# Kernel optimization log

Measured on AMD Instinct MI355X. Metric: run time of the kernel, lower is better.

Reference implementation:

```python
import jax, jax.numpy as jnp
import numpy as np

ALPHA = 0.1  # blend factor from init

def grid_sample_bilinear(tex, grid):
    # tex: [B,C,H,W]; grid: [B,Ho,Wo,2] with (x,y) in [-1,1].
    # Matches torch F.grid_sample(mode='bilinear', padding_mode='zeros', align_corners=False).
    B, C, H, W = tex.shape
    Ho, Wo = grid.shape[1], grid.shape[2]
    ix = ((grid[..., 0] + 1.0) * W - 1.0) * 0.5
    iy = ((grid[..., 1] + 1.0) * H - 1.0) * 0.5
    x0 = jnp.floor(ix); y0 = jnp.floor(iy)
    x1 = x0 + 1.0;      y1 = y0 + 1.0
    wx1 = ix - x0; wx0 = 1.0 - wx1
    wy1 = iy - y0; wy0 = 1.0 - wy1
    flat = tex.reshape(B, C, H * W).transpose(0, 2, 1)  # [B, H*W, C]

    def gather(xf, yf):
        valid = ((xf >= 0) & (xf < W) & (yf >= 0) & (yf < H)).astype(tex.dtype)
        xi = jnp.clip(xf.astype(jnp.int32), 0, W - 1)
        yi = jnp.clip(yf.astype(jnp.int32), 0, H - 1)
        idx = (yi * W + xi).reshape(B, Ho * Wo)
        v = jnp.take_along_axis(flat, idx[:, :, None], axis=1)  # [B, N, C]
        return v * valid.reshape(B, Ho * Wo)[:, :, None]

    w00 = (wx0 * wy0).reshape(B, -1)[:, :, None]
    w10 = (wx1 * wy0).reshape(B, -1)[:, :, None]
    w01 = (wx0 * wy1).reshape(B, -1)[:, :, None]
    w11 = (wx1 * wy1).reshape(B, -1)[:, :, None]
    out = (gather(x0, y0) * w00 + gather(x1, y0) * w10 +
           gather(x0, y1) * w01 + gather(x1, y1) * w11)  # [B, N, C]
    return out.reshape(B, Ho, Wo, C).transpose(0, 3, 1, 2)

def bicubic_grid_sample(tex, grid):
    # 5-tap Catmull-Rom approximation of bicubic filtering (matches BiCubicGridSample).
    B, C, H, W = tex.shape
    wsz = jnp.asarray([W, H], dtype=tex.dtype)
    rws = 1.0 / wsz
    uv = (grid + 1.0) * 0.5
    pos = uv * wsz
    cpos = jnp.floor(pos - 0.5) + 0.5
    f = pos - cpos; f2 = f * f; f3 = f2 * f
    w0 = -0.5 * f3 + f2 - 0.5 * f
    w1 = 1.5 * f3 - 2.5 * f2 + 1.0
    w2 = -1.5 * f3 + 2.0 * f2 + 0.5 * f
    w3 = 0.5 * f3 - 0.5 * f2
    w12 = w1 + w2
    tc12 = rws * (cpos + w2 / w12)
    tc0 = rws * (cpos - 1.0)
    tc3 = rws * (cpos + 2.0)

    def samp(u, v):
        uvg = jnp.stack((u, v), axis=-1)
        return grid_sample_bilinear(tex, (uvg - 0.5) * 2.0)  # UVToGrid

    # 5 taps in the plus pattern, with the per-tap scalar weights (alpha channel is a
    # constant 1 in the original, so the denominator is just the sum of the weights).
    k1 = w12[..., 0] * w0[..., 1]
    k2 = w0[..., 0] * w12[..., 1]
    k3 = w3[..., 0] * w12[..., 1]
    k4 = w12[..., 0] * w3[..., 1]
    k5 = w12[..., 0] * w12[..., 1]
    rgb = (samp(tc12[..., 0], tc0[..., 1]) * k1[:, None] +
           samp(tc0[..., 0], tc12[..., 1]) * k2[:, None] +
           samp(tc3[..., 0], tc12[..., 1]) * k3[:, None] +
           samp(tc12[..., 0], tc3[..., 1]) * k4[:, None] +
           samp(tc12[..., 0], tc12[..., 1]) * k5[:, None])
    denom = (k1 + k2 + k3 + k4 + k5)[:, None]
    return jnp.clip(rgb / denom, 0.0, 1.0)

def max_pool3(x):
    # 3x3 max pool, stride 1, padding 1 (SAME) on NCHW.
    return jax.lax.reduce_window(x, -jnp.inf, jax.lax.max,
                                 (1, 1, 3, 3), (1, 1, 1, 1), 'SAME')

def setup_inputs() -> dict:
    key = jax.random.key(0)
    k1, k2, k3 = jax.random.split(key, 3)
    B, C, H, W = 4, 3, 1080, 1920
    x = jax.random.uniform(k1, (B, C, H, W), dtype=jnp.float32)
    mv = jax.random.uniform(k2, (B, H, W, 2), dtype=jnp.float32)  # in [0,1) subset of [-1,1]
    history = jax.random.uniform(k3, (B, C, H, W), dtype=jnp.float32)
    return {"x": x, "mv": mv, "history": history}

def reference(x, mv, history):
    # TAA forward, steady-state (history present), use_bic=True, hist_clamp=True.
    rep = bicubic_grid_sample(history, mv)
    max_nh = max_pool3(x)
    min_nh = -max_pool3(-x)
    rep = jnp.minimum(jnp.maximum(rep, min_nh), max_nh)  # neighborhood clamp
    return ALPHA * x + (1.0 - ALPHA) * rep
```

## Files before the change

kernel.cpp:

```cpp
#include <hip/hip_runtime.h>

namespace {

constexpr int Bn = 4, Cn = 3, Hn = 1080, Wn = 1920;
constexpr int HW = Hn * Wn;
constexpr int Wt = Wn / 4;
constexpr int Ht = Hn / 4;
constexpr float kAlpha = 0.1f;
constexpr float kInv2047 = 1.0f / 2047.0f;
constexpr float kInv1023 = 1.0f / 1023.0f;

typedef float v2f __attribute__((ext_vector_type(2)));
typedef float v4f __attribute__((ext_vector_type(4)));
typedef unsigned int v4u __attribute__((ext_vector_type(4)));

__global__ __launch_bounds__(128)
void pack_tiled(const float* __restrict__ hist, unsigned int* __restrict__ packed)
{
    const int bid = blockIdx.x;
    const int b   = bid / (Ht * 15);
    const int r2  = bid - b * (Ht * 15);
    const int ty  = r2 / 15;
    const int txg = r2 - ty * 15;
    const int l   = threadIdx.x;
    const int tx  = txg * 32 + (l & 31);
    const int y   = ty * 4 + (l >> 5);
    const int x0  = tx * 4;

    const float* base = hist + (size_t)b * Cn * HW + (size_t)y * Wn + x0;
    const v4f r  = *(const v4f*)(base);
    const v4f g  = *(const v4f*)(base + HW);
    const v4f bl = *(const v4f*)(base + 2 * HW);

    v4u t;
    #pragma unroll
    for (int i = 0; i < 4; ++i) {
        const unsigned R  = (unsigned)(fminf(fmaxf(r[i],  0.0f), 1.0f) * 2047.0f + 0.5f);
        const unsigned G  = (unsigned)(fminf(fmaxf(g[i],  0.0f), 1.0f) * 2047.0f + 0.5f);
        const unsigned Bq = (unsigned)(fminf(fmaxf(bl[i], 0.0f), 1.0f) * 1023.0f + 0.5f);
        t[i] = (R << 21) | (G << 10) | Bq;
    }
    unsigned int* dst = packed + (size_t)b * HW + ((size_t)ty * Wt + tx) * 16 + (y & 3) * 4;
    *(v4u*)dst = t;
}

__device__ inline unsigned sel4(unsigned a, unsigned b, unsigned c, unsigned d, int s)
{
    const unsigned lo = (s & 1) ? b : a;
    const unsigned hi = (s & 1) ? d : c;
    return (s & 2) ? hi : lo;
}

__device__ inline void bicubic_gather(const unsigned int* __restrict__ pp,
                                      float gx, float gy, float rep[3])
{
    const float posx = (gx + 1.0f) * 0.5f * (float)Wn;
    const float posy = (gy + 1.0f) * 0.5f * (float)Hn;
    const float Xf = floorf(posx - 0.5f);
    const float Yf = floorf(posy - 0.5f);
    const float fx = posx - (Xf + 0.5f);
    const float fy = posy - (Yf + 0.5f);

    const float fx2 = fx * fx, fx3 = fx2 * fx;
    const float w0x = -0.5f * fx3 + fx2 - 0.5f * fx;
    const float w1x =  1.5f * fx3 - 2.5f * fx2 + 1.0f;
    const float w2x = -1.5f * fx3 + 2.0f * fx2 + 0.5f * fx;
    const float w3x =  0.5f * fx3 - 0.5f * fx2;
    const float w12x = w1x + w2x;
    const float bxr  = w2x / w12x;

    const float fy2 = fy * fy, fy3 = fy2 * fy;
    const float w0y = -0.5f * fy3 + fy2 - 0.5f * fy;
    const float w1y =  1.5f * fy3 - 2.5f * fy2 + 1.0f;
    const float w2y = -1.5f * fy3 + 2.0f * fy2 + 0.5f * fy;
    const float w3y =  0.5f * fy3 - 0.5f * fy2;
    const float w12y = w1y + w2y;
    const float byr  = w2y / w12y;

    const int X = (int)Xf;
    const int Y = (int)Yf;

    const float vxm1 = ((unsigned)(X - 1) < (unsigned)Wn) ? 1.0f : 0.0f;
    const float vx0  = ((unsigned)(X    ) < (unsigned)Wn) ? 1.0f : 0.0f;
    const float vx1  = ((unsigned)(X + 1) < (unsigned)Wn) ? 1.0f : 0.0f;
    const float vx2  = ((unsigned)(X + 2) < (unsigned)Wn) ? 1.0f : 0.0f;
    const float vym1 = ((unsigned)(Y - 1) < (unsigned)Hn) ? 1.0f : 0.0f;
    const float vy0  = ((unsigned)(Y    ) < (unsigned)Hn) ? 1.0f : 0.0f;
    const float vy1  = ((unsigned)(Y + 1) < (unsigned)Hn) ? 1.0f : 0.0f;
    const float vy2  = ((unsigned)(Y + 2) < (unsigned)Hn) ? 1.0f : 0.0f;

    const float k1 = w12x * w0y;
    const float k2 = w0x * w12y;
    const float k3 = w3x * w12y;
    const float k4 = w12x * w3y;
    const float k5 = w12x * w12y;
    const float inv_denom = 1.0f / (k1 + k2 + k3 + k4 + k5);

    const float wxl = 1.0f - bxr, wxh = bxr;
    const float wyl = 1.0f - byr, wyh = byr;

    const float wA = k1 * wxl * (vym1 * vx0);
    const float wB = k1 * wxh * (vym1 * vx1);
    const float wC = k2 * wyl * (vxm1 * vy0);
    const float wD = k2 * wyh * (vxm1 * vy1);
    const float wE = k3 * wyl * (vx2 * vy0);
    const float wF = k3 * wyh * (vx2 * vy1);
    const float wG = k4 * wxl * (vy2 * vx0);
    const float wH = k4 * wxh * (vy2 * vx1);
    const float wI = k5 * wxl * wyl * (vx0 * vy0);
    const float wJ = k5 * wxh * wyl * (vx1 * vy0);
    const float wK = k5 * wxl * wyh * (vx0 * vy1);
    const float wL = k5 * wxh * wyh * (vx1 * vy1);

    const int rYm = min(max(Y - 1, 0), Hn - 1);
    const int rY0 = min(max(Y,     0), Hn - 1);
    const int rY1 = min(max(Y + 1, 0), Hn - 1);
    const int rY2 = min(max(Y + 2, 0), Hn - 1);
    const int cX  = min(max(X,     0), Wn - 1);
    const int cX1 = min(max(X + 1, 0), Wn - 1);
    const int tx0 = min(max((X - 1) >> 2, 0), Wt - 1);
    const int tx1 = min(max((X + 2) >> 2, 0), Wt - 1);
    const int s1  = (X - 1) & 3;

    #define ROWBASE(rc, tx) ((((rc) >> 2) * Wt + (tx)) * 16 + ((rc) & 3) * 4)
    const v4u A0 = *(const v4u*)(pp + ROWBASE(rY0, tx0));
    const v4u A1 = *(const v4u*)(pp + ROWBASE(rY1, tx0));
    v4u B0 = {0, 0, 0, 0}, B1 = {0, 0, 0, 0};
    if (s1 != 0) {
        B0 = *(const v4u*)(pp + ROWBASE(rY0, tx1));
        B1 = *(const v4u*)(pp + ROWBASE(rY1, tx1));
    }
    const int txA = cX >> 2;
    const int sA  = cX & 3;
    const int sB  = cX1 & 3;
    const bool nb = (cX1 >> 2) != txA;
    const v4u Tm = *(const v4u*)(pp + ROWBASE(rYm, txA));
    const v4u T2 = *(const v4u*)(pp + ROWBASE(rY2, txA));
    unsigned um = 0, u2 = 0;
    if (nb) {
        um = pp[ROWBASE(rYm, txA + 1)];
        u2 = pp[ROWBASE(rY2, txA + 1)];
    }
    #undef ROWBASE

    const unsigned tA = sel4(Tm.x, Tm.y, Tm.z, Tm.w, sA);
    const unsigned tG = sel4(T2.x, T2.y, T2.z, T2.w, sA);
    const unsigned tB = nb ? um : sel4(Tm.x, Tm.y, Tm.z, Tm.w, sB);
    const unsigned tH = nb ? u2 : sel4(T2.x, T2.y, T2.z, T2.w, sB);

    const unsigned tC = sel4(A0.x, A0.y, A0.z, A0.w, s1);
    const unsigned tI = sel4(A0.y, A0.z, A0.w, B0.x, s1);
    const unsigned tJ = sel4(A0.z, A0.w, B0.x, B0.y, s1);
    const unsigned tE = sel4(A0.w, B0.x, B0.y, B0.z, s1);
    const unsigned tD = sel4(A1.x, A1.y, A1.z, A1.w, s1);
    const unsigned tK = sel4(A1.y, A1.z, A1.w, B1.x, s1);
    const unsigned tL = sel4(A1.z, A1.w, B1.x, B1.y, s1);
    const unsigned tF = sel4(A1.w, B1.x, B1.y, B1.z, s1);

    float accR = 0.0f, accG = 0.0f, accB = 0.0f;
#define TAA_TAP(w_, t_) {                                                   \
    accR = fmaf(w_, (float)((t_) >> 21),           accR);                   \
    accG = fmaf(w_, (float)(((t_) >> 10) & 2047u), accG);                   \
    accB = fmaf(w_, (float)((t_) & 1023u),         accB); }
    TAA_TAP(wA, tA) TAA_TAP(wB, tB) TAA_TAP(wC, tC) TAA_TAP(wD, tD)
    TAA_TAP(wE, tE) TAA_TAP(wF, tF) TAA_TAP(wG, tG) TAA_TAP(wH, tH)
    TAA_TAP(wI, tI) TAA_TAP(wJ, tJ) TAA_TAP(wK, tK) TAA_TAP(wL, tL)
#undef TAA_TAP
    rep[0] = accR * (kInv2047 * inv_denom);
    rep[1] = accG * (kInv2047 * inv_denom);
    rep[2] = accB * (kInv1023 * inv_denom);
}

__global__ __launch_bounds__(128)
void taa_main2(const float* __restrict__ xin,
               const v2f* __restrict__ mv,
               const unsigned int* __restrict__ packed,
               float* __restrict__ out)
{
    const int bid = blockIdx.x;
    const int b   = bid & 3;
    const int r   = bid >> 2;
    const int u   = r * 128 + threadIdx.x;
    const int py  = u / 960;
    const int P   = (u - py * 960) * 2;
    const int p   = py * Wn + P;

    const v4f gg = __builtin_nontemporal_load((const v4f*)&mv[(size_t)b * HW + p]);

    const unsigned int* __restrict__ pp = packed + (size_t)b * HW;
    float rep0[3], rep1[3];
    bicubic_gather(pp, gg.x, gg.y, rep0);
    bicubic_gather(pp, gg.z, gg.w, rep1);

    const int pym = max(py - 1, 0) * Wn;
    const int py0 = py * Wn;
    const int pyp = min(py + 1, Hn - 1) * Wn;
    const int lane = threadIdx.x & 63;

    float ctr0[3], ctr1[3];
    float mxlo[3], mxhi[3], mnlo[3], mnhi[3];
    #pragma unroll
    for (int c = 0; c < Cn; ++c) {
        const float* __restrict__ xp = xin + (size_t)(b * Cn + c) * HW;
        const v2f a = *(const v2f*)(xp + pym + P);
        const v2f m = *(const v2f*)(xp + py0 + P);
        const v2f z = *(const v2f*)(xp + pyp + P);
        ctr0[c] = m.x; ctr1[c] = m.y;
        mxlo[c] = fmaxf(fmaxf(a.x, m.x), z.x);
        mxhi[c] = fmaxf(fmaxf(a.y, m.y), z.y);
        mnlo[c] = fminf(fminf(a.x, m.x), z.x);
        mnhi[c] = fminf(fminf(a.y, m.y), z.y);
    }

    float lmx[3], lmn[3], rmx[3], rmn[3];
    #pragma unroll
    for (int c = 0; c < Cn; ++c) {
        lmx[c] = __shfl_up(mxhi[c], 1);
        lmn[c] = __shfl_up(mnhi[c], 1);
        rmx[c] = __shfl_down(mxlo[c], 1);
        rmn[c] = __shfl_down(mnlo[c], 1);
    }

    if (lane == 0 || lane == 63) {
        const int ex = (lane == 0) ? max(P - 1, 0) : min(P + 2, Wn - 1);
        #pragma unroll
        for (int c = 0; c < Cn; ++c) {
            const float* __restrict__ xp = xin + (size_t)(b * Cn + c) * HW;
            const float e0 = xp[pym + ex];
            const float e1 = xp[py0 + ex];
            const float e2 = xp[pyp + ex];
            const float emax = fmaxf(fmaxf(e0, e1), e2);
            const float emin = fminf(fminf(e0, e1), e2);
            if (lane == 0) { lmx[c] = emax; lmn[c] = emin; }
            else           { rmx[c] = emax; rmn[c] = emin; }
        }
    }

    #pragma unroll
    for (int c = 0; c < Cn; ++c) {
        const float mx0 = fmaxf(fmaxf(lmx[c], mxlo[c]), mxhi[c]);
        const float mn0 = fminf(fminf(lmn[c], mnlo[c]), mnhi[c]);
        const float mx1 = fmaxf(fmaxf(mxlo[c], mxhi[c]), rmx[c]);
        const float mn1 = fminf(fminf(mnlo[c], mnhi[c]), rmn[c]);

        float rv0 = fminf(fmaxf(rep0[c], 0.0f), 1.0f);
        float rv1 = fminf(fmaxf(rep1[c], 0.0f), 1.0f);
        rv0 = fminf(fmaxf(rv0, mn0), mx0);
        rv1 = fminf(fmaxf(rv1, mn1), mx1);

        v2f o;
        o.x = kAlpha * ctr0[c] + (1.0f - kAlpha) * rv0;
        o.y = kAlpha * ctr1[c] + (1.0f - kAlpha) * rv1;
        __builtin_nontemporal_store(o, (v2f*)&out[(size_t)(b * Cn + c) * HW + p]);
    }
}

__global__ __launch_bounds__(128)
void taa_fallback(const float* __restrict__ xin,
                  const v2f* __restrict__ mv,
                  const float* __restrict__ hist,
                  float* __restrict__ out)
{
    const int bid = blockIdx.x;
    const int b   = bid & 3;
    const int rr  = bid >> 2;
    const int py  = rr / 15;
    const int px  = (rr - py * 15) * 128 + threadIdx.x;
    const int p   = py * Wn + px;

    const v2f g = mv[(size_t)b * HW + p];
    const float posx = (g.x + 1.0f) * 0.5f * (float)Wn;
    const float posy = (g.y + 1.0f) * 0.5f * (float)Hn;
    const float Xf = floorf(posx - 0.5f);
    const float Yf = floorf(posy - 0.5f);
    const float fx = posx - (Xf + 0.5f);
    const float fy = posy - (Yf + 0.5f);
    const float fx2 = fx * fx, fx3 = fx2 * fx;
    const float w0x = -0.5f * fx3 + fx2 - 0.5f * fx;
    const float w1x =  1.5f * fx3 - 2.5f * fx2 + 1.0f;
    const float w2x = -1.5f * fx3 + 2.0f * fx2 + 0.5f * fx;
    const float w3x =  0.5f * fx3 - 0.5f * fx2;
    const float w12x = w1x + w2x, bxr = w2x / w12x;
    const float fy2 = fy * fy, fy3 = fy2 * fy;
    const float w0y = -0.5f * fy3 + fy2 - 0.5f * fy;
    const float w1y =  1.5f * fy3 - 2.5f * fy2 + 1.0f;
    const float w2y = -1.5f * fy3 + 2.0f * fy2 + 0.5f * fy;
    const float w3y =  0.5f * fy3 - 0.5f * fy2;
    const float w12y = w1y + w2y, byr = w2y / w12y;
    const int X = (int)Xf, Y = (int)Yf;
    const float vxm1 = ((unsigned)(X - 1) < (unsigned)Wn) ? 1.0f : 0.0f;
    const float vx0  = ((unsigned)(X    ) < (unsigned)Wn) ? 1.0f : 0.0f;
    const float vx1  = ((unsigned)(X + 1) < (unsigned)Wn) ? 1.0f : 0.0f;
    const float vx2  = ((unsigned)(X + 2) < (unsigned)Wn) ? 1.0f : 0.0f;
    const float vym1 = ((unsigned)(Y - 1) < (unsigned)Hn) ? 1.0f : 0.0f;
    const float vy0  = ((unsigned)(Y    ) < (unsigned)Hn) ? 1.0f : 0.0f;
    const float vy1  = ((unsigned)(Y + 1) < (unsigned)Hn) ? 1.0f : 0.0f;
    const float vy2  = ((unsigned)(Y + 2) < (unsigned)Hn) ? 1.0f : 0.0f;
    const float k1 = w12x * w0y, k2 = w0x * w12y, k3 = w3x * w12y;
    const float k4 = w12x * w3y, k5 = w12x * w12y;
    const float inv_denom = 1.0f / (k1 + k2 + k3 + k4 + k5);
    const float wxl = 1.0f - bxr, wxh = bxr, wyl = 1.0f - byr, wyh = byr;
    const float wA = k1 * wxl * (vym1 * vx0), wB = k1 * wxh * (vym1 * vx1);
    const float wC = k2 * wyl * (vxm1 * vy0), wD = k2 * wyh * (vxm1 * vy1);
    const float wE = k3 * wyl * (vx2 * vy0),  wF = k3 * wyh * (vx2 * vy1);
    const float wG = k4 * wxl * (vy2 * vx0),  wH = k4 * wxh * (vy2 * vx1);
    const float wI = k5 * wxl * wyl * (vx0 * vy0), wJ = k5 * wxh * wyl * (vx1 * vy0);
    const float wK = k5 * wxl * wyh * (vx0 * vy1), wL = k5 * wxh * wyh * (vx1 * vy1);
    const int cxm1 = min(max(X - 1, 0), Wn - 1), cx0 = min(max(X, 0), Wn - 1);
    const int cx1 = min(max(X + 1, 0), Wn - 1),  cx2 = min(max(X + 2, 0), Wn - 1);
    const int rym1 = min(max(Y - 1, 0), Hn - 1) * Wn, ry0 = min(max(Y, 0), Hn - 1) * Wn;
    const int ry1 = min(max(Y + 1, 0), Hn - 1) * Wn,  ry2 = min(max(Y + 2, 0), Hn - 1) * Wn;

    const int pym = max(py - 1, 0) * Wn;
    const int py0 = py * Wn;
    const int pyp = min(py + 1, Hn - 1) * Wn;
    const int pxm = max(px - 1, 0);
    const int pxp = min(px + 1, Wn - 1);

    #pragma unroll
    for (int c = 0; c < Cn; ++c) {
        const size_t plane = (size_t)(b * Cn + c) * HW;
        const float* __restrict__ hp = hist + plane;
        float acc = wA * hp[rym1 + cx0];
        acc = fmaf(wB, hp[rym1 + cx1], acc);
        acc = fmaf(wC, hp[ry0 + cxm1], acc);
        acc = fmaf(wD, hp[ry1 + cxm1], acc);
        acc = fmaf(wE, hp[ry0 + cx2], acc);
        acc = fmaf(wF, hp[ry1 + cx2], acc);
        acc = fmaf(wG, hp[ry2 + cx0], acc);
        acc = fmaf(wH, hp[ry2 + cx1], acc);
        acc = fmaf(wI, hp[ry0 + cx0], acc);
        acc = fmaf(wJ, hp[ry0 + cx1], acc);
        acc = fmaf(wK, hp[ry1 + cx0], acc);
        acc = fmaf(wL, hp[ry1 + cx1], acc);
        float rv = fminf(fmaxf(acc * inv_denom, 0.0f), 1.0f);

        const float* __restrict__ xp = xin + plane;
        const float r0a = xp[pym + pxm], r0b = xp[pym + px], r0c = xp[pym + pxp];
        const float r1a = xp[py0 + pxm], r1b = xp[py0 + px], r1c = xp[py0 + pxp];
        const float r2a = xp[pyp + pxm], r2b = xp[pyp + px], r2c = xp[pyp + pxp];
        const float mx = fmaxf(fmaxf(fmaxf(r0a, r0b), fmaxf(r0c, r1a)),
                               fmaxf(fmaxf(r1b, r1c), fmaxf(fmaxf(r2a, r2b), r2c)));
        const float mn = fminf(fminf(fminf(r0a, r0b), fminf(r0c, r1a)),
                               fminf(fminf(r1b, r1c), fminf(fminf(r2a, r2b), r2c)));
        rv = fminf(fmaxf(rv, mn), mx);
        out[plane + p] = kAlpha * r1b + (1.0f - kAlpha) * rv;
    }
}

}

extern "C" void kernel_launch(void* const* d_in, const int* in_sizes, int n_in,
                              void* d_out, int out_size, void* d_ws, size_t ws_size,
                              hipStream_t stream) {
    const float* x    = (const float*)d_in[0];
    const v2f*   mv   = (const v2f*)d_in[1];
    const float* hist = (const float*)d_in[2];
    float* outp = (float*)d_out;

    const size_t packed_bytes = (size_t)Bn * HW * 4;

    if (ws_size >= packed_bytes) {
        unsigned int* packed = (unsigned int*)d_ws;
        pack_tiled<<<Bn * Ht * 15, 128, 0, stream>>>(hist, packed);
        taa_main2<<<Bn * HW / 256, 128, 0, stream>>>(x, mv, packed, outp);
    } else {
        taa_fallback<<<(Wn / 128) * Hn * Bn, 128, 0, stream>>>(x, mv, hist, outp);
    }
}
```

Measured before the change: 444.5 us.

## Pack history into four phase-shifted copies for aligned vector bicubic gathers

Adds a packing kernel that writes four copies of the quantized history, each shifted by one pixel, so every row of the 4-wide bicubic footprint can be fetched with one aligned 16-byte load. A new main kernel handles two pixels per thread with wave shuffles for the 3x3 min/max neighborhood and nontemporal loads and stores. The cost is four times the workspace and pack write traffic, in exchange for fewer scattered gather loads. The path is used only when the workspace is large enough.

```diff
diff --git a/kernel.cpp b/kernel.cpp
--- a/kernel.cpp
+++ b/kernel.cpp
@@ -4,6 +4,7 @@
 
 constexpr int Bn = 4, Cn = 3, Hn = 1080, Wn = 1920;
 constexpr int HW = Hn * Wn;
+constexpr int Gt = Wn / 4;
 constexpr int Wt = Wn / 4;
 constexpr int Ht = Hn / 4;
 constexpr float kAlpha = 0.1f;
@@ -13,6 +14,237 @@
 typedef float v2f __attribute__((ext_vector_type(2)));
 typedef float v4f __attribute__((ext_vector_type(4)));
 typedef unsigned int v4u __attribute__((ext_vector_type(4)));
+
+__device__ inline unsigned quant_rgb(float r, float g, float b)
+{
+    const unsigned R  = (unsigned)(fminf(fmaxf(r, 0.0f), 1.0f) * 2047.0f + 0.5f);
+    const unsigned G  = (unsigned)(fminf(fmaxf(g, 0.0f), 1.0f) * 2047.0f + 0.5f);
+    const unsigned Bq = (unsigned)(fminf(fmaxf(b, 0.0f), 1.0f) * 1023.0f + 0.5f);
+    return (R << 21) | (G << 10) | Bq;
+}
+
+__global__ __launch_bounds__(256)
+void pack_phased(const float* __restrict__ hist, unsigned int* __restrict__ packed)
+{
+    const int tid = blockIdx.x * 256 + threadIdx.x;
+    const int g   = tid % Gt;
+    const int rem = tid / Gt;
+    const int y   = rem % Hn;
+    const int b   = rem / Hn;
+    const int x0  = g * 4;
+
+    const float* base = hist + (size_t)b * Cn * HW + (size_t)y * Wn + x0;
+    const v4f r  = *(const v4f*)(base);
+    const v4f gr = *(const v4f*)(base + HW);
+    const v4f bl = *(const v4f*)(base + 2 * HW);
+
+    const unsigned q0 = quant_rgb(r.x, gr.x, bl.x);
+    const unsigned q1 = quant_rgb(r.y, gr.y, bl.y);
+    const unsigned q2 = quant_rgb(r.z, gr.z, bl.z);
+    const unsigned q3 = quant_rgb(r.w, gr.w, bl.w);
+
+    unsigned n0 = __shfl_down(q0, 1);
+    unsigned n1 = __shfl_down(q1, 1);
+    unsigned n2 = __shfl_down(q2, 1);
+    const int lane = threadIdx.x & 63;
+    if (lane == 63 && g < Gt - 1) {
+        n0 = quant_rgb(base[4], base[4 + HW], base[4 + 2 * HW]);
+        n1 = quant_rgb(base[5], base[5 + HW], base[5 + 2 * HW]);
+        n2 = quant_rgb(base[6], base[6 + HW], base[6 + 2 * HW]);
+    }
+    if (g == Gt - 1) { n0 = q3; n1 = q3; n2 = q3; }
+
+    unsigned int* dst = packed + (size_t)b * 4 * HW + (size_t)y * Wn + x0;
+    *(v4u*)(dst)          = (v4u){q0, q1, q2, q3};
+    *(v4u*)(dst + HW)     = (v4u){q1, q2, q3, n0};
+    *(v4u*)(dst + 2 * HW) = (v4u){q2, q3, n0, n1};
+    *(v4u*)(dst + 3 * HW) = (v4u){q3, n0, n1, n2};
+}
+
+__device__ inline void bicubic_gather4(const unsigned int* __restrict__ pp,
+                                       float gx, float gy, float rep[3])
+{
+    const float posx = (gx + 1.0f) * 0.5f * (float)Wn;
+    const float posy = (gy + 1.0f) * 0.5f * (float)Hn;
+    const float Xf = floorf(posx - 0.5f);
+    const float Yf = floorf(posy - 0.5f);
+    const float fx = posx - (Xf + 0.5f);
+    const float fy = posy - (Yf + 0.5f);
+
+    const float fx2 = fx * fx, fx3 = fx2 * fx;
+    const float w0x = -0.5f * fx3 + fx2 - 0.5f * fx;
+    const float w1x =  1.5f * fx3 - 2.5f * fx2 + 1.0f;
+    const float w2x = -1.5f * fx3 + 2.0f * fx2 + 0.5f * fx;
+    const float w3x =  0.5f * fx3 - 0.5f * fx2;
+    const float w12x = w1x + w2x;
+    const float bxr  = w2x / w12x;
+
+    const float fy2 = fy * fy, fy3 = fy2 * fy;
+    const float w0y = -0.5f * fy3 + fy2 - 0.5f * fy;
+    const float w1y =  1.5f * fy3 - 2.5f * fy2 + 1.0f;
+    const float w2y = -1.5f * fy3 + 2.0f * fy2 + 0.5f * fy;
+    const float w3y =  0.5f * fy3 - 0.5f * fy2;
+    const float w12y = w1y + w2y;
+    const float byr  = w2y / w12y;
+
+    const int X = (int)Xf;
+    const int Y = (int)Yf;
+
+    const float vxm1 = ((unsigned)(X - 1) < (unsigned)Wn) ? 1.0f : 0.0f;
+    const float vx0  = ((unsigned)(X    ) < (unsigned)Wn) ? 1.0f : 0.0f;
+    const float vx1  = ((unsigned)(X + 1) < (unsigned)Wn) ? 1.0f : 0.0f;
+    const float vx2  = ((unsigned)(X + 2) < (unsigned)Wn) ? 1.0f : 0.0f;
+    const float vym1 = ((unsigned)(Y - 1) < (unsigned)Hn) ? 1.0f : 0.0f;
+    const float vy0  = ((unsigned)(Y    ) < (unsigned)Hn) ? 1.0f : 0.0f;
+    const float vy1  = ((unsigned)(Y + 1) < (unsigned)Hn) ? 1.0f : 0.0f;
+    const float vy2  = ((unsigned)(Y + 2) < (unsigned)Hn) ? 1.0f : 0.0f;
+
+    const float k1 = w12x * w0y;
+    const float k2 = w0x * w12y;
+    const float k3 = w3x * w12y;
+    const float k4 = w12x * w3y;
+    const float k5 = w12x * w12y;
+    const float inv_denom = 1.0f / (k1 + k2 + k3 + k4 + k5);
+
+    const float wxl = 1.0f - bxr, wxh = bxr;
+    const float wyl = 1.0f - byr, wyh = byr;
+
+    const float wA = k1 * wxl * (vym1 * vx0);
+    const float wB = k1 * wxh * (vym1 * vx1);
+    const float wC = k2 * wyl * (vxm1 * vy0);
+    const float wD = k2 * wyh * (vxm1 * vy1);
+    const float wE = k3 * wyl * (vx2 * vy0);
+    const float wF = k3 * wyh * (vx2 * vy1);
+    const float wG = k4 * wxl * (vy2 * vx0);
+    const float wH = k4 * wxh * (vy2 * vx1);
+    const float wI = k5 * wxl * wyl * (vx0 * vy0);
+    const float wJ = k5 * wxh * wyl * (vx1 * vy0);
+    const float wK = k5 * wxl * wyh * (vx0 * vy1);
+    const float wL = k5 * wxh * wyh * (vx1 * vy1);
+
+    const int W0 = X - 1;
+    const int k  = W0 & 3;
+    const int gq = min(max(W0 >> 2, 0), Gt - 1);
+
+    const int rYm = min(max(Y - 1, 0), Hn - 1) * Wn;
+    const int rY0 = min(max(Y,     0), Hn - 1) * Wn;
+    const int rY1 = min(max(Y + 1, 0), Hn - 1) * Wn;
+    const int rY2 = min(max(Y + 2, 0), Hn - 1) * Wn;
+
+    const unsigned int* bk = pp + (size_t)k * HW + gq * 4;
+    v4u R0 = *(const v4u*)(bk + rY0);
+    v4u R1 = *(const v4u*)(bk + rY1);
+    v4u Rm = *(const v4u*)(bk + rYm);
+    v4u R2 = *(const v4u*)(bk + rY2);
+
+    if (__builtin_expect(W0 < 0 && W0 > -4, 0)) {
+        const int c0 = min(max(W0,     0), Wn - 1);
+        const int c1 = min(max(W0 + 1, 0), Wn - 1);
+        const int c2 = min(max(W0 + 2, 0), Wn - 1);
+        const int c3 = min(max(W0 + 3, 0), Wn - 1);
+        R0 = (v4u){pp[rY0 + c0], pp[rY0 + c1], pp[rY0 + c2], pp[rY0 + c3]};
+        R1 = (v4u){pp[rY1 + c0], pp[rY1 + c1], pp[rY1 + c2], pp[rY1 + c3]};
+        Rm = (v4u){pp[rYm + c0], pp[rYm + c1], pp[rYm + c2], pp[rYm + c3]};
+        R2 = (v4u){pp[rY2 + c0], pp[rY2 + c1], pp[rY2 + c2], pp[rY2 + c3]};
+    }
+
+    float accR = 0.0f, accG = 0.0f, accB = 0.0f;
+#define TAA_TAP(w_, t_) {                                                   \
+    accR = fmaf(w_, (float)((t_) >> 21),           accR);                   \
+    accG = fmaf(w_, (float)(((t_) >> 10) & 2047u), accG);                   \
+    accB = fmaf(w_, (float)((t_) & 1023u),         accB); }
+    TAA_TAP(wA, Rm.y) TAA_TAP(wB, Rm.z) TAA_TAP(wC, R0.x) TAA_TAP(wD, R1.x)
+    TAA_TAP(wE, R0.w) TAA_TAP(wF, R1.w) TAA_TAP(wG, R2.y) TAA_TAP(wH, R2.z)
+    TAA_TAP(wI, R0.y) TAA_TAP(wJ, R0.z) TAA_TAP(wK, R1.y) TAA_TAP(wL, R1.z)
+#undef TAA_TAP
+    rep[0] = accR * (kInv2047 * inv_denom);
+    rep[1] = accG * (kInv2047 * inv_denom);
+    rep[2] = accB * (kInv1023 * inv_denom);
+}
+
+__global__ __launch_bounds__(128)
+void taa_main4(const float* __restrict__ xin,
+               const v2f* __restrict__ mv,
+               const unsigned int* __restrict__ packed,
+               float* __restrict__ out)
+{
+    const int bid = blockIdx.x;
+    const int b   = bid & 3;
+    const int r   = bid >> 2;
+    const int u   = r * 128 + threadIdx.x;
+    const int py  = u / 960;
+    const int P   = (u - py * 960) * 2;
+    const int p   = py * Wn + P;
+
+    const v4f gg = __builtin_nontemporal_load((const v4f*)&mv[(size_t)b * HW + p]);
+
+    const unsigned int* __restrict__ pp = packed + (size_t)b * 4 * HW;
+    float rep0[3], rep1[3];
+    bicubic_gather4(pp, gg.x, gg.y, rep0);
+    bicubic_gather4(pp, gg.z, gg.w, rep1);
+
+    const int pym = max(py - 1, 0) * Wn;
+    const int py0 = py * Wn;
+    const int pyp = min(py + 1, Hn - 1) * Wn;
+    const int lane = threadIdx.x & 63;
+
+    float ctr0[3], ctr1[3];
+    float mxlo[3], mxhi[3], mnlo[3], mnhi[3];
+    #pragma unroll
+    for (int c = 0; c < Cn; ++c) {
+        const float* __restrict__ xp = xin + (size_t)(b * Cn + c) * HW;
+        const v2f a = *(const v2f*)(xp + pym + P);
+        const v2f m = *(const v2f*)(xp + py0 + P);
+        const v2f z = *(const v2f*)(xp + pyp + P);
+        ctr0[c] = m.x; ctr1[c] = m.y;
+        mxlo[c] = fmaxf(fmaxf(a.x, m.x), z.x);
+        mxhi[c] = fmaxf(fmaxf(a.y, m.y), z.y);
+        mnlo[c] = fminf(fminf(a.x, m.x), z.x);
+        mnhi[c] = fminf(fminf(a.y, m.y), z.y);
+    }
+
+    float lmx[3], lmn[3], rmx[3], rmn[3];
+    #pragma unroll
+    for (int c = 0; c < Cn; ++c) {
+        lmx[c] = __shfl_up(mxhi[c], 1);
+        lmn[c] = __shfl_up(mnhi[c], 1);
+        rmx[c] = __shfl_down(mxlo[c], 1);
+        rmn[c] = __shfl_down(mnlo[c], 1);
+    }
+
+    if (lane == 0 || lane == 63) {
+        const int ex = (lane == 0) ? max(P - 1, 0) : min(P + 2, Wn - 1);
+        #pragma unroll
+        for (int c = 0; c < Cn; ++c) {
+            const float* __restrict__ xp = xin + (size_t)(b * Cn + c) * HW;
+            const float e0 = xp[pym + ex];
+            const float e1 = xp[py0 + ex];
+            const float e2 = xp[pyp + ex];
+            const float emax = fmaxf(fmaxf(e0, e1), e2);
+            const float emin = fminf(fminf(e0, e1), e2);
+            if (lane == 0) { lmx[c] = emax; lmn[c] = emin; }
+            else           { rmx[c] = emax; rmn[c] = emin; }
+        }
+    }
+
+    #pragma unroll
+    for (int c = 0; c < Cn; ++c) {
+        const float mx0 = fmaxf(fmaxf(lmx[c], mxlo[c]), mxhi[c]);
+        const float mn0 = fminf(fminf(lmn[c], mnlo[c]), mnhi[c]);
+        const float mx1 = fmaxf(fmaxf(mxlo[c], mxhi[c]), rmx[c]);
+        const float mn1 = fminf(fminf(mnlo[c], mnhi[c]), rmn[c]);
+
+        float rv0 = fminf(fmaxf(rep0[c], 0.0f), 1.0f);
+        float rv1 = fminf(fmaxf(rep1[c], 0.0f), 1.0f);
+        rv0 = fminf(fmaxf(rv0, mn0), mx0);
+        rv1 = fminf(fmaxf(rv1, mn1), mx1);
+
+        v2f o;
+        o.x = kAlpha * ctr0[c] + (1.0f - kAlpha) * rv0;
+        o.y = kAlpha * ctr1[c] + (1.0f - kAlpha) * rv1;
+        __builtin_nontemporal_store(o, (v2f*)&out[(size_t)(b * Cn + c) * HW + p]);
+    }
+}
 
 __global__ __launch_bounds__(128)
 void pack_tiled(const float* __restrict__ hist, unsigned int* __restrict__ packed)
@@ -34,12 +266,8 @@
 
     v4u t;
     #pragma unroll
-    for (int i = 0; i < 4; ++i) {
-        const unsigned R  = (unsigned)(fminf(fmaxf(r[i],  0.0f), 1.0f) * 2047.0f + 0.5f);
-        const unsigned G  = (unsigned)(fminf(fmaxf(g[i],  0.0f), 1.0f) * 2047.0f + 0.5f);
-        const unsigned Bq = (unsigned)(fminf(fmaxf(bl[i], 0.0f), 1.0f) * 1023.0f + 0.5f);
-        t[i] = (R << 21) | (G << 10) | Bq;
-    }
+    for (int i = 0; i < 4; ++i)
+        t[i] = quant_rgb(r[i], g[i], bl[i]);
     unsigned int* dst = packed + (size_t)b * HW + ((size_t)ty * Wt + tx) * 16 + (y & 3) * 4;
     *(v4u*)dst = t;
 }
@@ -358,9 +586,14 @@
     const float* hist = (const float*)d_in[2];
     float* outp = (float*)d_out;
 
+    const size_t phased_bytes = (size_t)Bn * 4 * HW * 4;
     const size_t packed_bytes = (size_t)Bn * HW * 4;
 
-    if (ws_size >= packed_bytes) {
+    if (ws_size >= phased_bytes) {
+        unsigned int* packed = (unsigned int*)d_ws;
+        pack_phased<<<Bn * Hn * Gt / 256, 256, 0, stream>>>(hist, packed);
+        taa_main4<<<Bn * HW / 256, 128, 0, stream>>>(x, mv, packed, outp);
+    } else if (ws_size >= packed_bytes) {
         unsigned int* packed = (unsigned int*)d_ws;
         pack_tiled<<<Bn * Ht * 15, 128, 0, stream>>>(hist, packed);
         taa_main2<<<Bn * HW / 256, 128, 0, stream>>>(x, mv, packed, outp);
```

Measured after the change: 610.1 us. 1.37x slower.

## Switch packed history to linear row-major layout with unaligned vector gathers

Applied to the files above, without the earlier changes.

Replaces the 4x4-tiled packed history buffer with a plain row-major packed buffer, offset by a small pad at both ends. The bicubic gather now reads the taps with unaligned 4-wide loads for the two center rows and 2-wide loads for the top and bottom rows. This removes the tile index math, the sel4 shuffles and the branchy extra loads. Out-of-range columns can now read wrapped or padded neighbours; these are expected to carry zero weight through the validity factors. The risks are split unaligned accesses and worse 2D cache locality for the random gathers.

```diff
diff --git a/kernel.cpp b/kernel.cpp
--- a/kernel.cpp
+++ b/kernel.cpp
@@ -4,55 +4,47 @@
 
 constexpr int Bn = 4, Cn = 3, Hn = 1080, Wn = 1920;
 constexpr int HW = Hn * Wn;
-constexpr int Wt = Wn / 4;
-constexpr int Ht = Hn / 4;
 constexpr float kAlpha = 0.1f;
 constexpr float kInv2047 = 1.0f / 2047.0f;
 constexpr float kInv1023 = 1.0f / 1023.0f;
+constexpr int kPad = 16;
 
 typedef float v2f __attribute__((ext_vector_type(2)));
 typedef float v4f __attribute__((ext_vector_type(4)));
 typedef unsigned int v4u __attribute__((ext_vector_type(4)));
-
-__global__ __launch_bounds__(128)
-void pack_tiled(const float* __restrict__ hist, unsigned int* __restrict__ packed)
-{
-    const int bid = blockIdx.x;
-    const int b   = bid / (Ht * 15);
-    const int r2  = bid - b * (Ht * 15);
-    const int ty  = r2 / 15;
-    const int txg = r2 - ty * 15;
-    const int l   = threadIdx.x;
-    const int tx  = txg * 32 + (l & 31);
-    const int y   = ty * 4 + (l >> 5);
-    const int x0  = tx * 4;
-
-    const float* base = hist + (size_t)b * Cn * HW + (size_t)y * Wn + x0;
-    const v4f r  = *(const v4f*)(base);
-    const v4f g  = *(const v4f*)(base + HW);
-    const v4f bl = *(const v4f*)(base + 2 * HW);
+typedef unsigned int v4u_u __attribute__((ext_vector_type(4), aligned(4)));
+typedef unsigned int v2u_u __attribute__((ext_vector_type(2), aligned(4)));
+
+__device__ inline unsigned quant_rgb(float r, float g, float b)
+{
+    const unsigned R  = (unsigned)(fminf(fmaxf(r, 0.0f), 1.0f) * 2047.0f + 0.5f);
+    const unsigned G  = (unsigned)(fminf(fmaxf(g, 0.0f), 1.0f) * 2047.0f + 0.5f);
+    const unsigned Bq = (unsigned)(fminf(fmaxf(b, 0.0f), 1.0f) * 1023.0f + 0.5f);
+    return (R << 21) | (G << 10) | Bq;
+}
+
+__global__ __launch_bounds__(256)
+void pack_linear(const float* __restrict__ hist, unsigned int* __restrict__ packed)
+{
+    const int tid = blockIdx.x * 256 + threadIdx.x;
+    const int b   = tid / (HW / 4);
+    const int r   = tid - b * (HW / 4);
+
+    const float* base = hist + (size_t)b * Cn * HW + (size_t)r * 4;
+    const v4f rr = *(const v4f*)(base);
+    const v4f gg = *(const v4f*)(base + HW);
+    const v4f bb = *(const v4f*)(base + 2 * HW);
 
     v4u t;
-    #pragma unroll
-    for (int i = 0; i < 4; ++i) {
-        const unsigned R  = (unsigned)(fminf(fmaxf(r[i],  0.0f), 1.0f) * 2047.0f + 0.5f);
-        const unsigned G  = (unsigned)(fminf(fmaxf(g[i],  0.0f), 1.0f) * 2047.0f + 0.5f);
-        const unsigned Bq = (unsigned)(fminf(fmaxf(bl[i], 0.0f), 1.0f) * 1023.0f + 0.5f);
-        t[i] = (R << 21) | (G << 10) | Bq;
-    }
-    unsigned int* dst = packed + (size_t)b * HW + ((size_t)ty * Wt + tx) * 16 + (y & 3) * 4;
-    *(v4u*)dst = t;
-}
-
-__device__ inline unsigned sel4(unsigned a, unsigned b, unsigned c, unsigned d, int s)
-{
-    const unsigned lo = (s & 1) ? b : a;
-    const unsigned hi = (s & 1) ? d : c;
-    return (s & 2) ? hi : lo;
-}
-
-__device__ inline void bicubic_gather(const unsigned int* __restrict__ pp,
-                                      float gx, float gy, float rep[3])
+    t.x = quant_rgb(rr.x, gg.x, bb.x);
+    t.y = quant_rgb(rr.y, gg.y, bb.y);
+    t.z = quant_rgb(rr.z, gg.z, bb.z);
+    t.w = quant_rgb(rr.w, gg.w, bb.w);
+    *(v4u*)(packed + (size_t)b * HW + (size_t)r * 4) = t;
+}
+
+__device__ inline void bicubic_gather_lin(const unsigned int* __restrict__ pp,
+                                          float gx, float gy, float rep[3])
 {
     const float posx = (gx + 1.0f) * 0.5f * (float)Wn;
     const float posy = (gy + 1.0f) * 0.5f * (float)Hn;
@@ -112,59 +104,25 @@
     const float wK = k5 * wxl * wyh * (vx0 * vy1);
     const float wL = k5 * wxh * wyh * (vx1 * vy1);
 
-    const int rYm = min(max(Y - 1, 0), Hn - 1);
-    const int rY0 = min(max(Y,     0), Hn - 1);
-    const int rY1 = min(max(Y + 1, 0), Hn - 1);
-    const int rY2 = min(max(Y + 2, 0), Hn - 1);
-    const int cX  = min(max(X,     0), Wn - 1);
-    const int cX1 = min(max(X + 1, 0), Wn - 1);
-    const int tx0 = min(max((X - 1) >> 2, 0), Wt - 1);
-    const int tx1 = min(max((X + 2) >> 2, 0), Wt - 1);
-    const int s1  = (X - 1) & 3;
-
-    #define ROWBASE(rc, tx) ((((rc) >> 2) * Wt + (tx)) * 16 + ((rc) & 3) * 4)
-    const v4u A0 = *(const v4u*)(pp + ROWBASE(rY0, tx0));
-    const v4u A1 = *(const v4u*)(pp + ROWBASE(rY1, tx0));
-    v4u B0 = {0, 0, 0, 0}, B1 = {0, 0, 0, 0};
-    if (s1 != 0) {
-        B0 = *(const v4u*)(pp + ROWBASE(rY0, tx1));
-        B1 = *(const v4u*)(pp + ROWBASE(rY1, tx1));
-    }
-    const int txA = cX >> 2;
-    const int sA  = cX & 3;
-    const int sB  = cX1 & 3;
-    const bool nb = (cX1 >> 2) != txA;
-    const v4u Tm = *(const v4u*)(pp + ROWBASE(rYm, txA));
-    const v4u T2 = *(const v4u*)(pp + ROWBASE(rY2, txA));
-    unsigned um = 0, u2 = 0;
-    if (nb) {
-        um = pp[ROWBASE(rYm, txA + 1)];
-        u2 = pp[ROWBASE(rY2, txA + 1)];
-    }
-    #undef ROWBASE
-
-    const unsigned tA = sel4(Tm.x, Tm.y, Tm.z, Tm.w, sA);
-    const unsigned tG = sel4(T2.x, T2.y, T2.z, T2.w, sA);
-    const unsigned tB = nb ? um : sel4(Tm.x, Tm.y, Tm.z, Tm.w, sB);
-    const unsigned tH = nb ? u2 : sel4(T2.x, T2.y, T2.z, T2.w, sB);
-
-    const unsigned tC = sel4(A0.x, A0.y, A0.z, A0.w, s1);
-    const unsigned tI = sel4(A0.y, A0.z, A0.w, B0.x, s1);
-    const unsigned tJ = sel4(A0.z, A0.w, B0.x, B0.y, s1);
-    const unsigned tE = sel4(A0.w, B0.x, B0.y, B0.z, s1);
-    const unsigned tD = sel4(A1.x, A1.y, A1.z, A1.w, s1);
-    const unsigned tK = sel4(A1.y, A1.z, A1.w, B1.x, s1);
-    const unsigned tL = sel4(A1.z, A1.w, B1.x, B1.y, s1);
-    const unsigned tF = sel4(A1.w, B1.x, B1.y, B1.z, s1);
+    const int W0  = X - 1;
+    const int rYm = min(max(Y - 1, 0), Hn - 1) * Wn;
+    const int rY0 = min(max(Y,     0), Hn - 1) * Wn;
+    const int rY1 = min(max(Y + 1, 0), Hn - 1) * Wn;
+    const int rY2 = min(max(Y + 2, 0), Hn - 1) * Wn;
+
+    const v4u_u R0 = *(const v4u_u*)(pp + rY0 + W0);
+    const v4u_u R1 = *(const v4u_u*)(pp + rY1 + W0);
+    const v2u_u Rm = *(const v2u_u*)(pp + rYm + X);
+    const v2u_u R2 = *(const v2u_u*)(pp + rY2 + X);
 
     float accR = 0.0f, accG = 0.0f, accB = 0.0f;
 #define TAA_TAP(w_, t_) {                                                   \
     accR = fmaf(w_, (float)((t_) >> 21),           accR);                   \
     accG = fmaf(w_, (float)(((t_) >> 10) & 2047u), accG);                   \
     accB = fmaf(w_, (float)((t_) & 1023u),         accB); }
-    TAA_TAP(wA, tA) TAA_TAP(wB, tB) TAA_TAP(wC, tC) TAA_TAP(wD, tD)
-    TAA_TAP(wE, tE) TAA_TAP(wF, tF) TAA_TAP(wG, tG) TAA_TAP(wH, tH)
-    TAA_TAP(wI, tI) TAA_TAP(wJ, tJ) TAA_TAP(wK, tK) TAA_TAP(wL, tL)
+    TAA_TAP(wA, Rm.x) TAA_TAP(wB, Rm.y) TAA_TAP(wC, R0.x) TAA_TAP(wD, R1.x)
+    TAA_TAP(wE, R0.w) TAA_TAP(wF, R1.w) TAA_TAP(wG, R2.x) TAA_TAP(wH, R2.y)
+    TAA_TAP(wI, R0.y) TAA_TAP(wJ, R0.z) TAA_TAP(wK, R1.y) TAA_TAP(wL, R1.z)
 #undef TAA_TAP
     rep[0] = accR * (kInv2047 * inv_denom);
     rep[1] = accG * (kInv2047 * inv_denom);
@@ -172,10 +130,10 @@
 }
 
 __global__ __launch_bounds__(128)
-void taa_main2(const float* __restrict__ xin,
-               const v2f* __restrict__ mv,
-               const unsigned int* __restrict__ packed,
-               float* __restrict__ out)
+void taa_main_lin(const float* __restrict__ xin,
+                  const v2f* __restrict__ mv,
+                  const unsigned int* __restrict__ packed,
+                  float* __restrict__ out)
 {
     const int bid = blockIdx.x;
     const int b   = bid & 3;
@@ -189,8 +147,8 @@
 
     const unsigned int* __restrict__ pp = packed + (size_t)b * HW;
     float rep0[3], rep1[3];
-    bicubic_gather(pp, gg.x, gg.y, rep0);
-    bicubic_gather(pp, gg.z, gg.w, rep1);
+    bicubic_gather_lin(pp, gg.x, gg.y, rep0);
+    bicubic_gather_lin(pp, gg.z, gg.w, rep1);
 
     const int pym = max(py - 1, 0) * Wn;
     const int py0 = py * Wn;
@@ -358,12 +316,12 @@
     const float* hist = (const float*)d_in[2];
     float* outp = (float*)d_out;
 
-    const size_t packed_bytes = (size_t)Bn * HW * 4;
-
-    if (ws_size >= packed_bytes) {
-        unsigned int* packed = (unsigned int*)d_ws;
-        pack_tiled<<<Bn * Ht * 15, 128, 0, stream>>>(hist, packed);
-        taa_main2<<<Bn * HW / 256, 128, 0, stream>>>(x, mv, packed, outp);
+    const size_t lin_bytes = ((size_t)Bn * HW + 2 * kPad) * 4;
+
+    if (ws_size >= lin_bytes) {
+        unsigned int* packed = (unsigned int*)d_ws + kPad;
+        pack_linear<<<Bn * HW / 4 / 256, 256, 0, stream>>>(hist, packed);
+        taa_main_lin<<<Bn * HW / 256, 128, 0, stream>>>(x, mv, packed, outp);
     } else {
         taa_fallback<<<(Wn / 128) * Hn * Bn, 128, 0, stream>>>(x, mv, hist, outp);
     }
```

Measured after the change: 419.8 us. -5.6%, faster.
